# Kernel optimization log

Measured on AMD Instinct MI355X. Metric: run time of the kernel, lower is better.

Reference implementation:

```python
import jax, jax.numpy as jnp
import numpy as np

D = 1024      # d_model
HD = 128      # shared k/v head dim == attn_expert_dim
EA = 8        # attention experts
KA = 2        # attention top-k
EF = 16       # ffn experts
KF = 2        # ffn top-k
FH = 512      # ffn expert hidden dim
MAXP = 64     # max relative positions
B, S = 4, 1024
EPS = 1e-5


def setup_inputs() -> dict:
    key = jax.random.key(0)
    ks = jax.random.split(key, 12)
    r = lambda i, shape, scale=0.02: jax.random.normal(ks[i], shape, jnp.float32) * scale
    return {
        "src": jax.random.normal(ks[0], (B, S, D), jnp.float32),
        "ln1_w": jnp.ones((D,), jnp.float32), "ln1_b": jnp.zeros((D,), jnp.float32),
        "ln2_w": jnp.ones((D,), jnp.float32), "ln2_b": jnp.zeros((D,), jnp.float32),
        "attn_gate_w": r(1, (D, EA)),
        "q_w": r(2, (EA, D, HD)), "q_b": jnp.zeros((EA, HD), jnp.float32),
        "k_w": r(3, (D, HD)), "k_b": jnp.zeros((HD,), jnp.float32),
        "v_w": r(4, (D, HD)), "v_b": jnp.zeros((HD,), jnp.float32),
        "o_w": r(5, (EA, HD, D)), "o_b": jnp.zeros((EA, D), jnp.float32),
        "rel_table": r(6, (2 * MAXP + 1, HD)),
        "ff_gate_w": r(7, (D, EF)),
        "ff_w1": r(8, (EF, D, FH)), "ff_b1": jnp.zeros((EF, FH), jnp.float32),
        "ff_w2": r(9, (EF, FH, D)), "ff_b2": jnp.zeros((EF, D), jnp.float32),
    }


def _layer_norm(x, w, b):
    mu = x.mean(-1, keepdims=True)
    var = ((x - mu) ** 2).mean(-1, keepdims=True)
    return (x - mu) * jax.lax.rsqrt(var + EPS) * w + b


def _topk_gates(logits, k):
    # top-k over router logits, softmax over the selected k, scatter to dense [.., E]
    top_vals, top_idx = jax.lax.top_k(logits, k)
    g = jax.nn.softmax(top_vals, axis=-1)
    onehot = jax.nn.one_hot(top_idx, logits.shape[-1], dtype=logits.dtype)  # [...,k,E]
    return jnp.einsum('...k,...ke->...e', g, onehot)


def _moa(x, gate_w, q_w, q_b, k_w, k_b, v_w, v_b, o_w, o_b, rel_table):
    # Mixture-of-attention: per-expert q/out projections, shared k/v, Shaw rel-pos.
    S_ = x.shape[1]
    gates = _topk_gates(x @ gate_w, KA)                                  # [B,S,EA]
    q = (jnp.einsum('bsd,edh->bseh', x, q_w) + q_b) * (HD ** -0.5)       # [B,S,EA,HD]
    k = x @ k_w + k_b                                                    # [B,S,HD]
    v = x @ v_w + v_b
    scores = jnp.einsum('bqeh,bkh->beqk', q, k)                          # [B,EA,S,S]
    rel_s = jnp.einsum('bqeh,rh->beqr', q, rel_table)                    # [B,EA,S,R]
    pos = jnp.arange(S_)
    rel_idx = jnp.clip(pos[None, :] - pos[:, None], -MAXP, MAXP) + MAXP  # [S,S]
    scores = scores + jnp.take_along_axis(rel_s, rel_idx[None, None], axis=-1)
    p = jax.nn.softmax(scores, axis=-1)
    ctx = jnp.einsum('beqk,bkh->bqeh', p, v)                             # [B,S,EA,HD]
    out = jnp.einsum('bqeh,ehd,bqe->bqd', ctx, o_w, gates)
    return out + jnp.einsum('bqe,ed->bqd', gates, o_b)


def _moe_ffn(x, gate_w, w1, b1, w2, b2):
    gates = _topk_gates(x @ gate_w, KF)                                  # [B,S,EF]
    h = jax.nn.relu(jnp.einsum('bsd,edh->bseh', x, w1) + b1)             # [B,S,EF,FH]
    out = jnp.einsum('bseh,ehd,bse->bsd', h, w2, gates)
    return out + jnp.einsum('bse,ed->bsd', gates, b2)


def reference(src, ln1_w, ln1_b, ln2_w, ln2_b, attn_gate_w, q_w, q_b, k_w, k_b,
              v_w, v_b, o_w, o_b, rel_table, ff_gate_w, ff_w1, ff_b1, ff_w2, ff_b2):
    # pre-LN residual block around MoE attention
    res = src
    xn = _layer_norm(src, ln1_w, ln1_b)
    x = res + _moa(xn, attn_gate_w, q_w, q_b, k_w, k_b, v_w, v_b, o_w, o_b, rel_table)
    # pre-LN residual block around MoE FFN
    res = x
    xn = _layer_norm(x, ln2_w, ln2_b)
    return res + _moe_ffn(xn, ff_gate_w, ff_w1, ff_b1, ff_w2, ff_b2)
```

## Files before the change

### kernel.cpp

```cpp
#include <hip/hip_runtime.h>

#define D 1024
#define HD 128
#define EA 8
#define EF 16
#define FH 512
#define MAXPOS 64
#define RNUM 129
#define RSTRIDE 132
#define SEQ 1024
#define NTOK 4096
#define NPAIR (NTOK * 2)
#define NPAD 8320
#define LN_EPS 1e-5f
#define QSCALE 0.08838834764831845f
#define BSTR 32
#define PROW 2048
#define NSPL 2

typedef __attribute__((ext_vector_type(8))) short bf16x8;
typedef __attribute__((ext_vector_type(4))) float f32x4;
typedef __attribute__((ext_vector_type(8))) unsigned short u16x8;

__device__ inline ushort f2b(float f) {
    union { float f; unsigned u; } v; v.f = f;
    unsigned r = (v.u + 0x7fffu + ((v.u >> 16) & 1u)) >> 16;
    return (ushort)r;
}
__device__ inline float b2f(ushort u) {
    union { unsigned u; float f; } v; v.u = (unsigned)u << 16; return v.f;
}

__device__ __forceinline__ void gll(const void* g, void* l) {
    __builtin_amdgcn_global_load_lds((const __attribute__((address_space(1))) void*)g,
                                     (__attribute__((address_space(3))) void*)l, 16, 0, 0);
}
__device__ __forceinline__ void wait_vm0()  { asm volatile("s_waitcnt vmcnt(0)" ::: "memory"); }
__device__ __forceinline__ void wait_vm3()  { asm volatile("s_waitcnt vmcnt(3)" ::: "memory"); }
__device__ __forceinline__ void wait_vm8()  { asm volatile("s_waitcnt vmcnt(8)" ::: "memory"); }
__device__ __forceinline__ void wait_vm16() { asm volatile("s_waitcnt vmcnt(16)" ::: "memory"); }
__device__ __forceinline__ void bar() { __builtin_amdgcn_s_barrier(); }

__device__ inline void mfma_step(const short* Asb, const short* Bsb,
                                 int wr, int wc, int m16, int q, f32x4 (&acc)[2][4]) {
    bf16x8 af[2], bfr[4];
#pragma unroll
    for (int i = 0; i < 2; i++) af[i] = *(const bf16x8*)&Asb[(wr + i * 16 + m16) * BSTR + q * 8];
#pragma unroll
    for (int j = 0; j < 4; j++) bfr[j] = *(const bf16x8*)&Bsb[(wc + j * 16 + m16) * BSTR + q * 8];
#pragma unroll
    for (int i = 0; i < 2; i++)
#pragma unroll
        for (int j = 0; j < 4; j++)
            acc[i][j] = __builtin_amdgcn_mfma_f32_16x16x32_bf16(af[i], bfr[j], acc[i][j], 0, 0, 0);
}

#define KLOOP(NK, AP, BP0, BP1, STRIDE)                                          \
    gll(AP, &As[0][w * 512]); gll(BP0, &Bs[0][w * 1024]); gll(BP1, &Bs[0][w * 1024 + 512]); \
    gll(AP + STRIDE, &As[1][w * 512]); gll(BP0 + STRIDE, &Bs[1][w * 1024]);      \
    gll(BP1 + STRIDE, &Bs[1][w * 1024 + 512]);                                   \
    {                                                                            \
        int cur = 0;                                                             \
        for (int k = 0; k < NK; k++) {                                           \
            if (k < NK - 1) wait_vm3(); else wait_vm0();                         \
            bar();                                                               \
            mfma_step(As[cur], Bs[cur], wr, wc, m16, q, acc);                    \
            if (k + 2 < NK) {                                                    \
                bar();                                                           \
                gll(AP + (k + 2) * STRIDE, &As[cur][w * 512]);                   \
                gll(BP0 + (k + 2) * STRIDE, &Bs[cur][w * 1024]);                 \
                gll(BP1 + (k + 2) * STRIDE, &Bs[cur][w * 1024 + 512]);           \
            }                                                                    \
            cur ^= 1;                                                            \
        }                                                                        \
    }

__global__ void ln_kernel(const float* __restrict__ x, const float* __restrict__ w,
                          const float* __restrict__ b, float* __restrict__ y,
                          ushort* __restrict__ yb) {
    int row = blockIdx.x;
    const float* xr = x + (size_t)row * D;
    float v[4];
    float s = 0.f, s2 = 0.f;
#pragma unroll
    for (int i = 0; i < 4; i++) {
        v[i] = xr[threadIdx.x + i * 256];
        s += v[i]; s2 += v[i] * v[i];
    }
#pragma unroll
    for (int off = 32; off; off >>= 1) { s += __shfl_down(s, off); s2 += __shfl_down(s2, off); }
    __shared__ float red0[4], red1[4];
    int wave = threadIdx.x >> 6, lane = threadIdx.x & 63;
    if (lane == 0) { red0[wave] = s; red1[wave] = s2; }
    __syncthreads();
    float ts = red0[0] + red0[1] + red0[2] + red0[3];
    float ts2 = red1[0] + red1[1] + red1[2] + red1[3];
    float mu = ts * (1.f / D);
    float var = ts2 * (1.f / D) - mu * mu;
    float inv = rsqrtf(var + LN_EPS);
#pragma unroll
    for (int i = 0; i < 4; i++) {
        int d = threadIdx.x + i * 256;
        float o = (v[i] - mu) * inv * w[d] + b[d];
        y[(size_t)row * D + d] = o;
        yb[(size_t)row * D + d] = f2b(o);
    }
}

template <int E>
__global__ void router_kernel(const float* __restrict__ xn, const float* __restrict__ gw,
                              int* __restrict__ idx, float* __restrict__ gate) {
    int t = blockIdx.x;
    int lane = threadIdx.x;
    float acc[E];
#pragma unroll
    for (int e = 0; e < E; e++) acc[e] = 0.f;
    const float* xr = xn + (size_t)t * D;
    for (int d = lane; d < D; d += 64) {
        float xv = xr[d];
#pragma unroll
        for (int e = 0; e < E; e++) acc[e] += xv * gw[d * E + e];
    }
#pragma unroll
    for (int e = 0; e < E; e++) {
#pragma unroll
        for (int off = 32; off; off >>= 1) acc[e] += __shfl_down(acc[e], off);
    }
    if (lane == 0) {
        float v0 = -1e30f, v1 = -1e30f;
        int i0 = 0, i1 = 0;
#pragma unroll
        for (int e = 0; e < E; e++) {
            float a = acc[e];
            if (a > v0) { v1 = v0; i1 = i0; v0 = a; i0 = e; }
            else if (a > v1) { v1 = a; i1 = e; }
        }
        float g0 = 1.f / (1.f + expf(v1 - v0));
        idx[t * 2] = i0; idx[t * 2 + 1] = i1;
        gate[t * 2] = g0; gate[t * 2 + 1] = 1.f - g0;
    }
}

__global__ void zero_meta(int* __restrict__ ameta, int* __restrict__ fmeta) {
    if (threadIdx.x < 105) ameta[threadIdx.x] = 0;
    if (threadIdx.x < 48) fmeta[threadIdx.x] = 0;
}

__global__ void abin_count(const int* __restrict__ aidx, int* __restrict__ meta) {
    int i = blockIdx.x * 256 + threadIdx.x;
    if (i < NPAIR) {
        int e = aidx[i];
        int b = (i >> 1) >> 10;
        atomicAdd(&meta[e * 4 + b], 1);
    }
}
__global__ void abin_scan(int* __restrict__ meta) {
    if (threadIdx.x == 0 && blockIdx.x == 0) {
        int s = 0;
        for (int bin = 0; bin < 32; bin++) {
            if ((bin & 3) == 0) meta[96 + (bin >> 2)] = s;
            meta[32 + bin] = s; meta[64 + bin] = s; s += meta[bin];
        }
        meta[96 + 8] = s;
    }
}
__global__ void abin_scatter(const int* __restrict__ aidx, int* __restrict__ meta,
                             int* __restrict__ list, int* __restrict__ inv) {
    int i = blockIdx.x * 256 + threadIdx.x;
    if (i < NPAIR) {
        int e = aidx[i];
        int b = (i >> 1) >> 10;
        int pos = atomicAdd(&meta[64 + e * 4 + b], 1);
        list[pos] = i;
        inv[i] = pos;
    }
}

__global__ void bin_count(const int* __restrict__ fidx, int* __restrict__ meta) {
    int i = blockIdx.x * 256 + threadIdx.x;
    if (i < NPAIR) atomicAdd(&meta[fidx[i]], 1);
}
__global__ void bin_scan(int* __restrict__ meta) {
    if (threadIdx.x == 0 && blockIdx.x == 0) {
        int s = 0;
        for (int e = 0; e < EF; e++) { meta[16 + e] = s; meta[32 + e] = s; s += meta[e]; }
    }
}
__global__ void bin_scatter(const int* __restrict__ fidx, int* __restrict__ meta,
                            int* __restrict__ list, int* __restrict__ inv) {
    int i = blockIdx.x * 256 + threadIdx.x;
    if (i < NPAIR) {
        int e = fidx[i];
        int pos = atomicAdd(&meta[32 + e], 1);
        list[pos] = i;
        inv[i] = pos;
    }
}

template <int R, int C>
__device__ __forceinline__ void convT_body(const float* __restrict__ src, ushort* __restrict__ dst) {
    int r0 = blockIdx.x * 32, c0 = blockIdx.y * 32;
    __shared__ float tile[32][33];
    int tx = threadIdx.x & 31, ty = threadIdx.x >> 5;
#pragma unroll
    for (int i = 0; i < 32; i += 8)
        tile[ty + i][tx] = src[(size_t)(r0 + ty + i) * C + c0 + tx];
    __syncthreads();
#pragma unroll
    for (int i = 0; i < 32; i += 8)
        dst[(size_t)(c0 + ty + i) * R + r0 + tx] = f2b(tile[tx][ty + i]);
}
template <int R, int C>
__global__ void convT_kernel(const float* __restrict__ in, ushort* __restrict__ out) {
    int e = blockIdx.z;
    convT_body<R, C>(in + (size_t)e * R * C, out + (size_t)e * C * R);
}
__global__ void convT_kv(const float* __restrict__ kw, const float* __restrict__ vw,
                         ushort* __restrict__ kwt, ushort* __restrict__ vwt) {
    if (blockIdx.z == 0) convT_body<1024, 128>(kw, kwt);
    else                 convT_body<1024, 128>(vw, vwt);
}

__global__ void conv_kernel(const float* __restrict__ in, ushort* __restrict__ out, int n) {
    int i = blockIdx.x * 256 + threadIdx.x;
    if (i < n) out[i] = f2b(in[i]);
}

__global__ __launch_bounds__(256) void kv_mfma(
    const ushort* __restrict__ xnb, const ushort* __restrict__ kwt,
    const ushort* __restrict__ vwt, float* __restrict__ kpart, float* __restrict__ vpart) {
    const ushort* W = blockIdx.z ? vwt : kwt;
    float* outp = blockIdx.z ? vpart : kpart;
    int m0 = blockIdx.x * 64;
    int s = blockIdx.y;
    int kbase = s * 512;
    __shared__ __align__(16) short As[2][64 * BSTR];
    __shared__ __align__(16) short Bs[2][128 * BSTR];
    int tid = threadIdx.x, w = tid >> 6, lane = tid & 63;
    int sr = lane >> 2, sc = (lane & 3) * 8;
    const ushort* ap = xnb + (size_t)(m0 + w * 16 + sr) * D + kbase + sc;
    const ushort* bp0 = W + (size_t)(w * 32 + sr) * D + kbase + sc;
    const ushort* bp1 = bp0 + (size_t)16 * D;
    int wr = (w >> 1) * 32, wc = (w & 1) * 64;
    int m16 = lane & 15, q = lane >> 4;
    f32x4 acc[2][4] = {};
    KLOOP(16, ap, bp0, bp1, 32)
#pragma unroll
    for (int i = 0; i < 2; i++)
#pragma unroll
        for (int r = 0; r < 4; r++) {
            int m = m0 + wr + i * 16 + q * 4 + r;
#pragma unroll
            for (int j = 0; j < 4; j++)
                outp[((size_t)s * NTOK + m) * HD + wc + j * 16 + m16] = acc[i][j][r];
        }
}

__global__ void kv_reduce(const float* __restrict__ kpart, const float* __restrict__ vpart,
                          const float* __restrict__ kb, const float* __restrict__ vb,
                          ushort* __restrict__ kb16, float* __restrict__ vbf) {
    int t = blockIdx.x, h = threadIdx.x;
    float ka = kb[h], va = vb[h];
#pragma unroll
    for (int s = 0; s < NSPL; s++) {
        ka += kpart[((size_t)s * NTOK + t) * HD + h];
        va += vpart[((size_t)s * NTOK + t) * HD + h];
    }
    kb16[(size_t)t * HD + h] = f2b(ka);
    vbf[(size_t)t * HD + h] = va;
}

__global__ __launch_bounds__(256) void q_mfma(
    const ushort* __restrict__ xnb, const ushort* __restrict__ qwt,
    const int* __restrict__ meta, const int* __restrict__ list, float* __restrict__ qpart) {
    int e = blockIdx.z;
    int o = meta[96 + e], c = meta[97 + e] - o;
    int m0 = blockIdx.x * 64;
    if (m0 >= c) return;
    int s = blockIdx.y;
    int kbase = s * 512;
    __shared__ __align__(16) short As[2][64 * BSTR];
    __shared__ __align__(16) short Bs[2][128 * BSTR];
    int tid = threadIdx.x, w = tid >> 6, lane = tid & 63;
    int sr = lane >> 2, sc = (lane & 3) * 8;
    int ri = o + m0 + w * 16 + sr; if (ri > NPAIR - 1) ri = NPAIR - 1;
    const ushort* ap = xnb + (size_t)(list[ri] >> 1) * D + kbase + sc;
    const ushort* bp0 = qwt + (size_t)e * HD * D + (size_t)(w * 32 + sr) * D + kbase + sc;
    const ushort* bp1 = bp0 + (size_t)16 * D;
    int wr = (w >> 1) * 32, wc = (w & 1) * 64;
    int m16 = lane & 15, q = lane >> 4;
    f32x4 acc[2][4] = {};
    KLOOP(16, ap, bp0, bp1, 32)
#pragma unroll
    for (int i = 0; i < 2; i++)
#pragma unroll
        for (int r = 0; r < 4; r++) {
            int pos = o + m0 + wr + i * 16 + q * 4 + r;
            if (pos < o + c) {
#pragma unroll
                for (int j = 0; j < 4; j++)
                    qpart[((size_t)s * NPAD + pos) * HD + wc + j * 16 + m16] = acc[i][j][r];
            }
        }
}

__global__ void q_reduce(const float* __restrict__ qpart, const float* __restrict__ qb,
                         const int* __restrict__ aidx, const int* __restrict__ list,
                         ushort* __restrict__ Qg) {
    int pos = blockIdx.x, h = threadIdx.x;
    int e = aidx[list[pos]];
    float a = qb[e * HD + h];
#pragma unroll
    for (int s = 0; s < NSPL; s++) a += qpart[((size_t)s * NPAD + pos) * HD + h];
    Qg[(size_t)pos * HD + h] = f2b(a * QSCALE);
}

__global__ __launch_bounds__(256) void rel_mfma(
    const ushort* __restrict__ Qg, const ushort* __restrict__ relb,
    float* __restrict__ R) {
    int m0 = blockIdx.x * 64;
    int n0 = blockIdx.y * 128;
    __shared__ __align__(16) short As[2][64 * BSTR];
    __shared__ __align__(16) short Bs[2][128 * BSTR];
    int tid = threadIdx.x, w = tid >> 6, lane = tid & 63;
    int sr = lane >> 2, sc = (lane & 3) * 8;
    const ushort* ap = Qg + (size_t)(m0 + w * 16 + sr) * HD + sc;
    int r0 = n0 + w * 32 + sr;      if (r0 > RNUM - 1) r0 = RNUM - 1;
    int r1 = n0 + w * 32 + 16 + sr; if (r1 > RNUM - 1) r1 = RNUM - 1;
    const ushort* bp0 = relb + (size_t)r0 * HD + sc;
    const ushort* bp1 = relb + (size_t)r1 * HD + sc;
    int wr = (w >> 1) * 32, wc = (w & 1) * 64;
    int m16 = lane & 15, q = lane >> 4;
    f32x4 acc[2][4] = {};
    KLOOP(4, ap, bp0, bp1, 32)
#pragma unroll
    for (int i = 0; i < 2; i++)
#pragma unroll
        for (int r = 0; r < 4; r++) {
            int pos = m0 + wr + i * 16 + q * 4 + r;
#pragma unroll
            for (int j = 0; j < 4; j++) {
                int n = n0 + wc + j * 16 + m16;
                if (n < RNUM) R[(size_t)pos * RSTRIDE + n] = acc[i][j][r];
            }
        }
}

__global__ __launch_bounds__(256) void flash_attn(
    const ushort* __restrict__ Qg, const ushort* __restrict__ kb16,
    const ushort* __restrict__ vt16, const float* __restrict__ Rbuf,
    const int* __restrict__ meta, const int* __restrict__ list,
    const float* __restrict__ aga, ushort* __restrict__ ctx16) {
    int bin = blockIdx.z;
    int o = meta[32 + bin], c = meta[bin];
    int m0 = blockIdx.x * 64;
    if (m0 >= c) return;
    int b = bin & 3;
    __shared__ __align__(16) ushort QP[64 * 128];
    __shared__ __align__(16) ushort KV[2][128 * 128];
    int tid = threadIdx.x, w = tid >> 6, lane = tid & 63;
    int m16 = lane & 15, q = lane >> 4;
    int srow4 = lane >> 4, scol = lane & 15;

#pragma unroll
    for (int t = 0; t < 4; t++) {
        int row = w * 16 + t * 4 + srow4;
        int rg = o + m0 + row; if (rg > NPAIR - 1) rg = NPAIR - 1;
        gll(Qg + (size_t)rg * HD + ((scol ^ (row & 7)) * 8), &QP[(w * 16 + t * 4) * 128]);
    }
#pragma unroll
    for (int u = 0; u < 8; u++) {
        int row = w * 32 + u * 4 + srow4;
        gll(kb16 + ((size_t)b * SEQ + row) * HD + ((scol ^ (row & 7)) * 8), &KV[0][(w * 32 + u * 4) * 128]);
    }
#pragma unroll
    for (int u = 0; u < 8; u++) {
        int row = w * 32 + u * 4 + srow4;
        gll(vt16 + ((size_t)b * HD + row) * SEQ + ((scol ^ (row & 7)) * 8), &KV[1][(w * 32 + u * 4) * 128]);
    }

    int lid[4]; int qpos[4]; const float* Rrow[4];
#pragma unroll
    for (int r = 0; r < 4; r++) {
        int pos = o + m0 + w * 16 + q * 4 + r;
        int pc = pos < NPAIR ? pos : NPAIR - 1;
        lid[r] = list[pc];
        qpos[r] = (lid[r] >> 1) & (SEQ - 1);
        Rrow[r] = Rbuf + (size_t)pc * RSTRIDE;
    }
    float m_run[4], l_run[4];
#pragma unroll
    for (int r = 0; r < 4; r++) { m_run[r] = -1e30f; l_run[r] = 0.f; }
    f32x4 acc_o[8];
#pragma unroll
    for (int j = 0; j < 8; j++) acc_o[j] = (f32x4){0.f, 0.f, 0.f, 0.f};

    wait_vm16();
    bf16x8 qf[4];
#pragma unroll
    for (int kk = 0; kk < 4; kk++)
        qf[kk] = *(const bf16x8*)&QP[(w * 16 + m16) * 128 + (((q + 4 * kk) ^ (m16 & 7)) * 8)];

    for (int kt = 0; kt < 8; kt++) {
        wait_vm8();
        bar();
        f32x4 s_[8];
#pragma unroll
        for (int j = 0; j < 8; j++) s_[j] = (f32x4){0.f, 0.f, 0.f, 0.f};
#pragma unroll
        for (int kk = 0; kk < 4; kk++) {
#pragma unroll
            for (int j = 0; j < 8; j++) {
                bf16x8 bb = *(const bf16x8*)&KV[0][(j * 16 + m16) * 128 + (((q + 4 * kk) ^ (m16 & 7)) * 8)];
                s_[j] = __builtin_amdgcn_mfma_f32_16x16x32_bf16(qf[kk], bb, s_[j], 0, 0, 0);
            }
        }
        float mloc[4] = {-1e30f, -1e30f, -1e30f, -1e30f};
#pragma unroll
        for (int j = 0; j < 8; j++) {
            int key = kt * 128 + j * 16 + m16;
#pragma unroll
            for (int r = 0; r < 4; r++) {
                int rix = key - qpos[r];
                rix = (rix < -MAXPOS ? -MAXPOS : (rix > MAXPOS ? MAXPOS : rix)) + MAXPOS;
                float vv = s_[j][r] + Rrow[r][rix];
                s_[j][r] = vv;
                mloc[r] = fmaxf(mloc[r], vv);
            }
        }
#pragma unroll
        for (int off = 8; off; off >>= 1)
#pragma unroll
            for (int r = 0; r < 4; r++) mloc[r] = fmaxf(mloc[r], __shfl_xor(mloc[r], off, 16));
        float scale_[4], lloc[4] = {0.f, 0.f, 0.f, 0.f};
#pragma unroll
        for (int r = 0; r < 4; r++) {
            float mn = fmaxf(m_run[r], mloc[r]);
            scale_[r] = __expf(m_run[r] - mn);
            m_run[r] = mn;
        }
#pragma unroll
        for (int j = 0; j < 8; j++) {
#pragma unroll
            for (int r = 0; r < 4; r++) {
                float p = __expf(s_[j][r] - m_run[r]);
                lloc[r] += p;
                int row = q * 4 + r;
                QP[(w * 16 + row) * 128 + ((j * 16 + m16) ^ ((row & 7) * 8))] = f2b(p);
            }
        }
#pragma unroll
        for (int off = 8; off; off >>= 1)
#pragma unroll
            for (int r = 0; r < 4; r++) lloc[r] += __shfl_xor(lloc[r], off, 16);
#pragma unroll
        for (int r = 0; r < 4; r++) l_run[r] = l_run[r] * scale_[r] + lloc[r];
#pragma unroll
        for (int j = 0; j < 8; j++)
#pragma unroll
            for (int r = 0; r < 4; r++) acc_o[j][r] *= scale_[r];
        bar();
        if (kt < 7) {
#pragma unroll
            for (int u = 0; u < 8; u++) {
                int row = w * 32 + u * 4 + srow4;
                gll(kb16 + ((size_t)b * SEQ + (kt + 1) * 128 + row) * HD + ((scol ^ (row & 7)) * 8),
                    &KV[0][(w * 32 + u * 4) * 128]);
            }
            wait_vm8();
        } else {
            wait_vm0();
        }
        bar();
#pragma unroll
        for (int kk = 0; kk < 4; kk++) {
            bf16x8 pf = *(const bf16x8*)&QP[(w * 16 + m16) * 128 + (((q + 4 * kk) ^ (m16 & 7)) * 8)];
#pragma unroll
            for (int j = 0; j < 8; j++) {
                bf16x8 vv = *(const bf16x8*)&KV[1][(j * 16 + m16) * 128 + (((q + 4 * kk) ^ (m16 & 7)) * 8)];
                acc_o[j] = __builtin_amdgcn_mfma_f32_16x16x32_bf16(pf, vv, acc_o[j], 0, 0, 0);
            }
        }
        bar();
        if (kt < 7) {
#pragma unroll
            for (int u = 0; u < 8; u++) {
                int row = w * 32 + u * 4 + srow4;
                gll(vt16 + ((size_t)b * HD + row) * SEQ + (kt + 1) * 128 + ((scol ^ (row & 7)) * 8),
                    &KV[1][(w * 32 + u * 4) * 128]);
            }
        }
    }
#pragma unroll
    for (int r = 0; r < 4; r++) {
        int pos = o + m0 + w * 16 + q * 4 + r;
        if (pos < o + c) {
            float g = aga[lid[r]] / l_run[r];
#pragma unroll
            for (int j = 0; j < 8; j++)
                ctx16[(size_t)pos * HD + j * 16 + m16] = f2b(acc_o[j][r] * g);
        }
    }
}

__global__ __launch_bounds__(256) void o_mfma(
    const ushort* __restrict__ ctx16, const ushort* __restrict__ owt,
    const int* __restrict__ meta, ushort* __restrict__ Ofb) {
    int e = blockIdx.z;
    int o = meta[96 + e], c = meta[97 + e] - o;
    int m0 = blockIdx.x * 64;
    if (m0 >= c) return;
    int n0 = blockIdx.y * 128;
    __shared__ __align__(16) short As[2][64 * BSTR];
    __shared__ __align__(16) short Bs[2][128 * BSTR];
    int tid = threadIdx.x, w = tid >> 6, lane = tid & 63;
    int sr = lane >> 2, sc = (lane & 3) * 8;
    int ar = o + m0 + w * 16 + sr; if (ar > NPAIR - 1) ar = NPAIR - 1;
    const ushort* ap = ctx16 + (size_t)ar * HD + sc;
    const ushort* bp0 = owt + (size_t)e * D * HD + (size_t)(n0 + w * 32 + sr) * HD + sc;
    const ushort* bp1 = bp0 + (size_t)16 * HD;
    int wr = (w >> 1) * 32, wc = (w & 1) * 64;
    int m16 = lane & 15, q = lane >> 4;
    f32x4 acc[2][4] = {};
    KLOOP(4, ap, bp0, bp1, 32)
#pragma unroll
    for (int i = 0; i < 2; i++)
#pragma unroll
        for (int r = 0; r < 4; r++) {
            int pos = o + m0 + wr + i * 16 + q * 4 + r;
            if (pos < o + c) {
#pragma unroll
                for (int j = 0; j < 4; j++)
                    Ofb[(size_t)pos * D + n0 + wc + j * 16 + m16] = f2b(acc[i][j][r]);
            }
        }
}

__global__ void attn_combine(const float* __restrict__ src, const float* __restrict__ ob,
                             const int* __restrict__ aidx, const float* __restrict__ aga,
                             const int* __restrict__ ainv, const ushort* __restrict__ Ofb,
                             float* __restrict__ x1) {
    int t = blockIdx.x, tid = threadIdx.x;
    int e0 = aidx[t * 2], e1 = aidx[t * 2 + 1];
    float g0 = aga[t * 2], g1 = aga[t * 2 + 1];
    int p0 = ainv[t * 2], p1 = ainv[t * 2 + 1];
#pragma unroll
    for (int i = 0; i < 4; i++) {
        int d = tid + i * 256;
        x1[(size_t)t * D + d] = src[(size_t)t * D + d]
                              + g0 * ob[e0 * D + d] + g1 * ob[e1 * D + d]
                              + b2f(Ofb[(size_t)p0 * D + d]) + b2f(Ofb[(size_t)p1 * D + d]);
    }
}

__global__ __launch_bounds__(256) void ffn_mfma1(
    const ushort* __restrict__ xnb2, const ushort* __restrict__ w1t,
    const float* __restrict__ b1, const int* __restrict__ meta,
    const int* __restrict__ list, const float* __restrict__ fga,
    ushort* __restrict__ Hb) {
    int e = blockIdx.z;
    int o = meta[16 + e], c = meta[e];
    int m0 = blockIdx.x * 64;
    if (m0 >= c) return;
    int n0 = blockIdx.y * 128;
    __shared__ __align__(16) short As[2][64 * BSTR];
    __shared__ __align__(16) short Bs[2][128 * BSTR];
    int tid = threadIdx.x, w = tid >> 6, lane = tid & 63;
    int sr = lane >> 2, sc = (lane & 3) * 8;
    int ri = o + m0 + w * 16 + sr; if (ri > NPAIR - 1) ri = NPAIR - 1;
    const ushort* ap = xnb2 + (size_t)(list[ri] >> 1) * D + sc;
    const ushort* bp0 = w1t + ((size_t)e * FH + n0 + w * 32 + sr) * D + sc;
    const ushort* bp1 = bp0 + (size_t)16 * D;
    int wr = (w >> 1) * 32, wc = (w & 1) * 64;
    int m16 = lane & 15, q = lane >> 4;
    f32x4 acc[2][4] = {};
    KLOOP(32, ap, bp0, bp1, 32)
#pragma unroll
    for (int i = 0; i < 2; i++)
#pragma unroll
        for (int r = 0; r < 4; r++) {
            int pos = o + m0 + wr + i * 16 + q * 4 + r;
            if (pos < o + c) {
                float g = fga[list[pos]];
#pragma unroll
                for (int j = 0; j < 4; j++) {
                    int n = n0 + wc + j * 16 + m16;
                    Hb[(size_t)pos * FH + n] = f2b(g * fmaxf(acc[i][j][r] + b1[e * FH + n], 0.f));
                }
            }
        }
}

__global__ __launch_bounds__(256) void ffn_mfma2(
    const ushort* __restrict__ Hb, const ushort* __restrict__ w2t,
    const int* __restrict__ meta, ushort* __restrict__ Of2b) {
    int e = blockIdx.z;
    int o = meta[16 + e], c = meta[e];
    int m0 = blockIdx.x * 64;
    if (m0 >= c) return;
    int n0 = blockIdx.y * 128;
    __shared__ __align__(16) short As[2][64 * BSTR];
    __shared__ __align__(16) short Bs[2][128 * BSTR];
    int tid = threadIdx.x, w = tid >> 6, lane = tid & 63;
    int sr = lane >> 2, sc = (lane & 3) * 8;
    int ar = o + m0 + w * 16 + sr; if (ar > NPAIR - 1) ar = NPAIR - 1;
    const ushort* ap = Hb + (size_t)ar * FH + sc;
    const ushort* bp0 = w2t + ((size_t)e * D + n0 + w * 32 + sr) * FH + sc;
    const ushort* bp1 = bp0 + (size_t)16 * FH;
    int wr = (w >> 1) * 32, wc = (w & 1) * 64;
    int m16 = lane & 15, q = lane >> 4;
    f32x4 acc[2][4] = {};
    KLOOP(16, ap, bp0, bp1, 32)
#pragma unroll
    for (int i = 0; i < 2; i++)
#pragma unroll
        for (int r = 0; r < 4; r++) {
            int pos = o + m0 + wr + i * 16 + q * 4 + r;
            if (pos < o + c) {
#pragma unroll
                for (int j = 0; j < 4; j++)
                    Of2b[(size_t)pos * D + n0 + wc + j * 16 + m16] = f2b(acc[i][j][r]);
            }
        }
}

__global__ void ffn_combine(const float* __restrict__ x1, const float* __restrict__ b2,
                            const int* __restrict__ fidx, const float* __restrict__ fga,
                            const int* __restrict__ finv, const ushort* __restrict__ Of2b,
                            float* __restrict__ out) {
    int t = blockIdx.x, tid = threadIdx.x;
    int e0 = fidx[t * 2], e1 = fidx[t * 2 + 1];
    float g0 = fga[t * 2], g1 = fga[t * 2 + 1];
    int p0 = finv[t * 2], p1 = finv[t * 2 + 1];
#pragma unroll
    for (int i = 0; i < 4; i++) {
        int d = tid + i * 256;
        out[(size_t)t * D + d] = x1[(size_t)t * D + d]
                               + g0 * b2[e0 * D + d] + g1 * b2[e1 * D + d]
                               + b2f(Of2b[(size_t)p0 * D + d]) + b2f(Of2b[(size_t)p1 * D + d]);
    }
}

extern "C" void kernel_launch(void* const* d_in, const int* in_sizes, int n_in,
                              void* d_out, int out_size, void* d_ws, size_t ws_size,
                              hipStream_t stream) {
    const float* src   = (const float*)d_in[0];
    const float* ln1_w = (const float*)d_in[1];
    const float* ln1_b = (const float*)d_in[2];
    const float* ln2_w = (const float*)d_in[3];
    const float* ln2_b = (const float*)d_in[4];
    const float* agw   = (const float*)d_in[5];
    const float* qw    = (const float*)d_in[6];
    const float* qb    = (const float*)d_in[7];
    const float* kw    = (const float*)d_in[8];
    const float* kb    = (const float*)d_in[9];
    const float* vw    = (const float*)d_in[10];
    const float* vb    = (const float*)d_in[11];
    const float* ow    = (const float*)d_in[12];
    const float* ob    = (const float*)d_in[13];
    const float* rel   = (const float*)d_in[14];
    const float* fgw   = (const float*)d_in[15];
    const float* w1    = (const float*)d_in[16];
    const float* b1    = (const float*)d_in[17];
    const float* w2    = (const float*)d_in[18];
    const float* b2    = (const float*)d_in[19];
    float* out = (float*)d_out;

    char* p = (char*)d_ws;
    float* xn1  = (float*)p; p += (size_t)NTOK * D * 4;
    float* x1   = (float*)p; p += (size_t)NTOK * D * 4;
    char*  sreg = p;         p += (size_t)NPAD * SEQ * 4;
    ushort* Ofb  = (ushort*)sreg;
    ushort* w1t  = (ushort*)sreg;
    ushort* w2t  = (ushort*)(sreg + (size_t)16777216);
    char*  reg  = p;         p += (size_t)NPAD * 128 * 6 + (size_t)NPAIR * RSTRIDE * 4;
    ushort* ctx16 = (ushort*)reg;
    ushort* Qg   = (ushort*)(reg + (size_t)NPAD * 128 * 4);
    float*  Rbuf = (float*)(reg + (size_t)NPAD * 128 * 6);
    ushort* Hb   = (ushort*)reg;
    char*  arena = p;        p += (size_t)4 * NPAD * 128 * 4;
    float*  kpart = (float*)arena;
    float*  vpart = (float*)(arena + (size_t)NSPL * NTOK * HD * 4);
    float*  qpart = (float*)arena;
    ushort* Of2b  = (ushort*)arena;
    ushort* kb16 = (ushort*)p; p += (size_t)NTOK * HD * 2;
    float* vbf  = (float*)p; p += (size_t)NTOK * HD * 4;
    ushort* vt16 = (ushort*)p; p += (size_t)NTOK * HD * 2;
    ushort* kwt = (ushort*)p; p += (size_t)HD * D * 2;
    ushort* vwt = (ushort*)p; p += (size_t)HD * D * 2;
    ushort* qwt = (ushort*)p; p += (size_t)EA * HD * D * 2;
    ushort* owt = (ushort*)p; p += (size_t)EA * D * HD * 2;
    ushort* relb = (ushort*)p; p += (size_t)RNUM * HD * 2 + 256;
    int*   aidx = (int*)p;   p += NPAIR * 4;
    float* aga  = (float*)p; p += NPAIR * 4;
    int*   fidx = (int*)p;   p += NPAIR * 4;
    float* fga  = (float*)p; p += NPAIR * 4;
    int*   ameta = (int*)p;  p += 128 * 4;
    int*   alist = (int*)p;  p += NPAIR * 4;
    int*   ainv = (int*)p;   p += NPAIR * 4;
    int*   fmeta = (int*)p;  p += 64 * 4;
    int*   flist = (int*)p;  p += NPAIR * 4;
    int*   finv = (int*)p;   p += NPAIR * 4;
    ushort* xnb = (ushort*)p; p += (size_t)NTOK * D * 2;
    float* xn2 = xn1;

    zero_meta<<<1, 128, 0, stream>>>(ameta, fmeta);
    ln_kernel<<<NTOK, 256, 0, stream>>>(src, ln1_w, ln1_b, xn1, xnb);
    router_kernel<EA><<<NTOK, 64, 0, stream>>>(xn1, agw, aidx, aga);
    abin_count<<<NPAIR / 256, 256, 0, stream>>>(aidx, ameta);
    abin_scan<<<1, 64, 0, stream>>>(ameta);
    abin_scatter<<<NPAIR / 256, 256, 0, stream>>>(aidx, ameta, alist, ainv);
    convT_kv<<<dim3(32, 4, 2), 256, 0, stream>>>(kw, vw, kwt, vwt);
    convT_kernel<1024, 128><<<dim3(32, 4, EA), 256, 0, stream>>>(qw, qwt);
    convT_kernel<128, 1024><<<dim3(4, 32, EA), 256, 0, stream>>>(ow, owt);
    conv_kernel<<<(RNUM * HD + 255) / 256, 256, 0, stream>>>(rel, relb, RNUM * HD);
    kv_mfma<<<dim3(64, NSPL, 2), 256, 0, stream>>>(xnb, kwt, vwt, kpart, vpart);
    kv_reduce<<<NTOK, 128, 0, stream>>>(kpart, vpart, kb, vb, kb16, vbf);
    convT_kernel<1024, 128><<<dim3(32, 4, 4), 256, 0, stream>>>(vbf, vt16);
    q_mfma<<<dim3(40, NSPL, EA), 256, 0, stream>>>(xnb, qwt, ameta, alist, qpart);
    q_reduce<<<NPAIR, 128, 0, stream>>>(qpart, qb, aidx, alist, Qg);
    rel_mfma<<<dim3(NPAIR / 64, 2), 256, 0, stream>>>(Qg, relb, Rbuf);
    flash_attn<<<dim3(12, 1, 32), 256, 0, stream>>>(Qg, kb16, vt16, Rbuf, ameta, alist, aga, ctx16);
    o_mfma<<<dim3(40, 8, EA), 256, 0, stream>>>(ctx16, owt, ameta, Ofb);
    attn_combine<<<NTOK, 256, 0, stream>>>(src, ob, aidx, aga, ainv, Ofb, x1);

    ln_kernel<<<NTOK, 256, 0, stream>>>(x1, ln2_w, ln2_b, xn2, xnb);
    router_kernel<EF><<<NTOK, 64, 0, stream>>>(xn2, fgw, fidx, fga);
    bin_count<<<NPAIR / 256, 256, 0, stream>>>(fidx, fmeta);
    bin_scan<<<1, 64, 0, stream>>>(fmeta);
    bin_scatter<<<NPAIR / 256, 256, 0, stream>>>(fidx, fmeta, flist, finv);
    convT_kernel<1024, 512><<<dim3(32, 16, EF), 256, 0, stream>>>(w1, w1t);
    convT_kernel<512, 1024><<<dim3(16, 32, EF), 256, 0, stream>>>(w2, w2t);
    ffn_mfma1<<<dim3(20, 4, EF), 256, 0, stream>>>(xnb, w1t, b1, fmeta, flist, fga, Hb);
    ffn_mfma2<<<dim3(20, 8, EF), 256, 0, stream>>>(Hb, w2t, fmeta, Of2b);
    ffn_combine<<<NTOK, 256, 0, stream>>>(x1, b2, fidx, fga, finv, Of2b, out);
}
```

Before: 516.7 us.

## Split flash attention over key blocks and merge partials in a combine kernel

The flash attention kernel now splits the 1024 keys into NKV=4 chunks along a new grid dimension. Each block writes unnormalized partial outputs plus running max and sum to scratch buffers, and a new flash_combine kernel merges them with log-sum-exp rescaling, then applies the gate and converts to bf16. This is meant to fix low occupancy, since the old grid had only about 12x32 mostly-sparse blocks. In exchange it adds fp32 partial-output traffic, one more kernel launch, and repeated Q loads per split.

```diff
diff --git a/kernel.cpp b/kernel.cpp
--- a/kernel.cpp
+++ b/kernel.cpp
@@ -15,8 +15,8 @@
 #define LN_EPS 1e-5f
 #define QSCALE 0.08838834764831845f
 #define BSTR 32
-#define PROW 2048
 #define NSPL 2
+#define NKV 4
 
 typedef __attribute__((ext_vector_type(8))) short bf16x8;
 typedef __attribute__((ext_vector_type(4))) float f32x4;
@@ -350,12 +350,14 @@
     const ushort* __restrict__ Qg, const ushort* __restrict__ kb16,
     const ushort* __restrict__ vt16, const float* __restrict__ Rbuf,
     const int* __restrict__ meta, const int* __restrict__ list,
-    const float* __restrict__ aga, ushort* __restrict__ ctx16) {
+    float* __restrict__ Opart, float* __restrict__ mbuf, float* __restrict__ lbuf) {
     int bin = blockIdx.z;
     int o = meta[32 + bin], c = meta[bin];
     int m0 = blockIdx.x * 64;
     if (m0 >= c) return;
     int b = bin & 3;
+    int half = blockIdx.y;
+    int TK0 = half * (8 / NKV);
     __shared__ __align__(16) ushort QP[64 * 128];
     __shared__ __align__(16) ushort KV[2][128 * 128];
     int tid = threadIdx.x, w = tid >> 6, lane = tid & 63;
@@ -371,21 +373,22 @@
 #pragma unroll
     for (int u = 0; u < 8; u++) {
         int row = w * 32 + u * 4 + srow4;
-        gll(kb16 + ((size_t)b * SEQ + row) * HD + ((scol ^ (row & 7)) * 8), &KV[0][(w * 32 + u * 4) * 128]);
+        gll(kb16 + ((size_t)b * SEQ + TK0 * 128 + row) * HD + ((scol ^ (row & 7)) * 8),
+            &KV[0][(w * 32 + u * 4) * 128]);
     }
 #pragma unroll
     for (int u = 0; u < 8; u++) {
         int row = w * 32 + u * 4 + srow4;
-        gll(vt16 + ((size_t)b * HD + row) * SEQ + ((scol ^ (row & 7)) * 8), &KV[1][(w * 32 + u * 4) * 128]);
-    }
-
-    int lid[4]; int qpos[4]; const float* Rrow[4];
+        gll(vt16 + ((size_t)b * HD + row) * SEQ + TK0 * 128 + ((scol ^ (row & 7)) * 8),
+            &KV[1][(w * 32 + u * 4) * 128]);
+    }
+
+    int qpos[4]; const float* Rrow[4];
 #pragma unroll
     for (int r = 0; r < 4; r++) {
         int pos = o + m0 + w * 16 + q * 4 + r;
         int pc = pos < NPAIR ? pos : NPAIR - 1;
-        lid[r] = list[pc];
-        qpos[r] = (lid[r] >> 1) & (SEQ - 1);
+        qpos[r] = (list[pc] >> 1) & (SEQ - 1);
         Rrow[r] = Rbuf + (size_t)pc * RSTRIDE;
     }
     float m_run[4], l_run[4];
@@ -401,7 +404,9 @@
     for (int kk = 0; kk < 4; kk++)
         qf[kk] = *(const bf16x8*)&QP[(w * 16 + m16) * 128 + (((q + 4 * kk) ^ (m16 & 7)) * 8)];
 
-    for (int kt = 0; kt < 8; kt++) {
+#pragma unroll
+    for (int t2 = 0; t2 < 8 / NKV; t2++) {
+        int kt = TK0 + t2;
         wait_vm8();
         bar();
         f32x4 s_[8];
@@ -460,7 +465,7 @@
 #pragma unroll
             for (int r = 0; r < 4; r++) acc_o[j][r] *= scale_[r];
         bar();
-        if (kt < 7) {
+        if (t2 < 8 / NKV - 1) {
 #pragma unroll
             for (int u = 0; u < 8; u++) {
                 int row = w * 32 + u * 4 + srow4;
@@ -482,7 +487,7 @@
             }
         }
         bar();
-        if (kt < 7) {
+        if (t2 < 8 / NKV - 1) {
 #pragma unroll
             for (int u = 0; u < 8; u++) {
                 int row = w * 32 + u * 4 + srow4;
@@ -495,12 +500,33 @@
     for (int r = 0; r < 4; r++) {
         int pos = o + m0 + w * 16 + q * 4 + r;
         if (pos < o + c) {
-            float g = aga[lid[r]] / l_run[r];
+            if (m16 == 0) {
+                mbuf[(size_t)half * NPAD + pos] = m_run[r];
+                lbuf[(size_t)half * NPAD + pos] = l_run[r];
+            }
 #pragma unroll
             for (int j = 0; j < 8; j++)
-                ctx16[(size_t)pos * HD + j * 16 + m16] = f2b(acc_o[j][r] * g);
-        }
-    }
+                Opart[((size_t)half * NPAD + pos) * HD + j * 16 + m16] = acc_o[j][r];
+        }
+    }
+}
+
+__global__ void flash_combine(const float* __restrict__ Opart, const float* __restrict__ mbuf,
+                              const float* __restrict__ lbuf, const float* __restrict__ aga,
+                              const int* __restrict__ list, ushort* __restrict__ ctx16) {
+    int pos = blockIdx.x, h = threadIdx.x;
+    float M = -1e30f;
+#pragma unroll
+    for (int i = 0; i < NKV; i++) M = fmaxf(M, mbuf[(size_t)i * NPAD + pos]);
+    float L = 0.f, O = 0.f;
+#pragma unroll
+    for (int i = 0; i < NKV; i++) {
+        float e = __expf(mbuf[(size_t)i * NPAD + pos] - M);
+        L += lbuf[(size_t)i * NPAD + pos] * e;
+        O += Opart[((size_t)i * NPAD + pos) * HD + h] * e;
+    }
+    float g = aga[list[pos]] / L;
+    ctx16[(size_t)pos * HD + h] = f2b(O * g);
 }
 
 __global__ __launch_bounds__(256) void o_mfma(
@@ -682,6 +708,7 @@
     float*  kpart = (float*)arena;
     float*  vpart = (float*)(arena + (size_t)NSPL * NTOK * HD * 4);
     float*  qpart = (float*)arena;
+    float*  Opart = (float*)arena;
     ushort* Of2b  = (ushort*)arena;
     ushort* kb16 = (ushort*)p; p += (size_t)NTOK * HD * 2;
     float* vbf  = (float*)p; p += (size_t)NTOK * HD * 4;
@@ -702,6 +729,8 @@
     int*   flist = (int*)p;  p += NPAIR * 4;
     int*   finv = (int*)p;   p += NPAIR * 4;
     ushort* xnb = (ushort*)p; p += (size_t)NTOK * D * 2;
+    float* mbuf = (float*)p; p += (size_t)NKV * NPAD * 4;
+    float* lbuf = (float*)p; p += (size_t)NKV * NPAD * 4;
     float* xn2 = xn1;
 
     zero_meta<<<1, 128, 0, stream>>>(ameta, fmeta);
@@ -720,7 +749,9 @@
     q_mfma<<<dim3(40, NSPL, EA), 256, 0, stream>>>(xnb, qwt, ameta, alist, qpart);
     q_reduce<<<NPAIR, 128, 0, stream>>>(qpart, qb, aidx, alist, Qg);
     rel_mfma<<<dim3(NPAIR / 64, 2), 256, 0, stream>>>(Qg, relb, Rbuf);
-    flash_attn<<<dim3(12, 1, 32), 256, 0, stream>>>(Qg, kb16, vt16, Rbuf, ameta, alist, aga, ctx16);
+    flash_attn<<<dim3(12, NKV, 32), 256, 0, stream>>>(Qg, kb16, vt16, Rbuf, ameta, alist,
+                                                      Opart, mbuf, lbuf);
+    flash_combine<<<NPAIR, 128, 0, stream>>>(Opart, mbuf, lbuf, aga, alist, ctx16);
     o_mfma<<<dim3(40, 8, EA), 256, 0, stream>>>(ctx16, owt, ameta, Ofb);
     attn_combine<<<NTOK, 256, 0, stream>>>(src, ob, aidx, aga, ainv, Ofb, x1);
 
```

Result: faster. 489.9 us (-5.2%).
